# Kernel optimization log

Hardware: AMD Instinct MI355X
Metric: run time of the kernel (lower is better)

## Reference

```python
import jax, jax.numpy as jnp
import numpy as np

MODEL_DIM = 2048
NUM_HEADS = 16
NUM_KV_HEADS = 4
HEAD_DIM = MODEL_DIM // NUM_HEADS  # 128
ROPE_BASE = 10000.0
LOCAL_WINDOW = 1024
EPS = 1.1920929e-07  # torch.finfo(float32).eps, F.rms_norm default
NEG = -1e30


def setup_inputs() -> dict:
    key = jax.random.key(0)
    ks = jax.random.split(key, 5)
    s = 0.02
    return {
        "x": jax.random.normal(ks[0], (1, 4096, MODEL_DIM), jnp.float32),
        "Wq": jax.random.normal(ks[1], (MODEL_DIM, MODEL_DIM), jnp.float32) * s,
        "Wk": jax.random.normal(ks[2], (NUM_KV_HEADS * HEAD_DIM, MODEL_DIM), jnp.float32) * s,
        "Wv": jax.random.normal(ks[3], (NUM_KV_HEADS * HEAD_DIM, MODEL_DIM), jnp.float32) * s,
        "Wo": jax.random.normal(ks[4], (MODEL_DIM, MODEL_DIM), jnp.float32) * s,
    }


def _rms_norm(x):
    return x * jax.lax.rsqrt(jnp.mean(x * x, axis=-1, keepdims=True) + EPS)


def _rope_tables(seqlen, dtype):
    inv_freq = 1.0 / (ROPE_BASE ** (jnp.arange(0, HEAD_DIM, 2, dtype=jnp.float32) / HEAD_DIM))
    freqs = jnp.arange(seqlen, dtype=jnp.float32)[:, None] * inv_freq[None, :]  # [S, hd/2]
    return jnp.cos(freqs).astype(dtype), jnp.sin(freqs).astype(dtype)


def _apply_rope(x, cos, sin):
    # x: [B, H, S, hd]; cos/sin: [S, hd/2]
    half = x.shape[-1] // 2
    x1, x2 = x[..., :half], x[..., half:]
    c = cos[None, None, :, :]
    s = sin[None, None, :, :]
    return jnp.concatenate((x1 * c + x2 * s, x2 * c - x1 * s), axis=-1)


def reference(x, Wq, Wk, Wv, Wo):
    B, S, _ = x.shape
    G = NUM_HEADS // NUM_KV_HEADS
    q = (x @ Wq.T).reshape(B, S, NUM_HEADS, HEAD_DIM).transpose(0, 2, 1, 3)
    k = (x @ Wk.T).reshape(B, S, NUM_KV_HEADS, HEAD_DIM).transpose(0, 2, 1, 3)
    v = (x @ Wv.T).reshape(B, S, NUM_KV_HEADS, HEAD_DIM).transpose(0, 2, 1, 3)
    q = _rms_norm(q)
    k = _rms_norm(k)
    cos, sin = _rope_tables(S, q.dtype)
    q = _apply_rope(q, cos, sin)
    k = _apply_rope(k, cos, sin)
    # GQA: expand kv heads to match query heads
    k = jnp.repeat(k, G, axis=1)  # [B, H, S, hd]
    v = jnp.repeat(v, G, axis=1)
    scale = 1.0 / np.sqrt(HEAD_DIM)
    scores = jnp.einsum("bhqd,bhkd->bhqk", q, k) * scale  # [B, H, S, S]
    idx = jnp.arange(S)
    causal = idx[None, :] <= idx[:, None]
    in_window = idx[None, :] > idx[:, None] - LOCAL_WINDOW
    allowed = causal & in_window  # [S, S]
    scores = jnp.where(allowed[None, None, :, :], scores, NEG)
    probs = jax.nn.softmax(scores, axis=-1)
    y = jnp.einsum("bhqk,bhkd->bhqd", probs, v)  # [B, H, S, hd]
    y = y.transpose(0, 2, 1, 3).reshape(B, S, MODEL_DIM)
    return y @ Wo.T
```

## Files before the change

kernel.cpp:

```cpp
#include <hip/hip_runtime.h>

typedef short bf16x8 __attribute__((ext_vector_type(8)));
typedef float f32x4 __attribute__((ext_vector_type(4)));

__device__ __forceinline__ ushort f2b(float f) {
  union { float f; unsigned u; } v; v.f = f;
  unsigned r = v.u + 0x7FFF + ((v.u >> 16) & 1);
  return (ushort)(r >> 16);
}
__device__ __forceinline__ float b2f(ushort u) {
  union { unsigned u; float f; } v; v.u = ((unsigned)u) << 16;
  return v.f;
}
__device__ __forceinline__ unsigned cvtpk(float lo, float hi) {
  unsigned r;
  asm volatile("v_cvt_pk_bf16_f32 %0, %1, %2" : "=v"(r) : "v"(lo), "v"(hi));
  return r;
}
__device__ __forceinline__ f32x4 mfma16(bf16x8 a, bf16x8 b, f32x4 c) {
  return __builtin_amdgcn_mfma_f32_16x16x32_bf16(a, b, c, 0, 0, 0);
}

#define GLD_LDS16(g, l) \
  __builtin_amdgcn_global_load_lds((const __attribute__((address_space(1))) void*)(g), \
                                   (__attribute__((address_space(3))) void*)(l), 16, 0, 0)

__global__ __launch_bounds__(256) void cast_all(const float* __restrict__ x,
                                                const float* __restrict__ wq,
                                                const float* __restrict__ wk,
                                                const float* __restrict__ wv,
                                                const float* __restrict__ wo,
                                                ushort* __restrict__ xb,
                                                ushort* __restrict__ wqkvb,
                                                ushort* __restrict__ wob) {
  const long i = (long)blockIdx.x * 256 + threadIdx.x;
  const float* src;
  ushort* dst;
  long j;
  if (i < 2097152) {
    src = x; j = i; dst = xb;
  } else if (i < 3145728) {
    src = wq; j = i - 2097152; dst = wqkvb;
  } else if (i < 3407872) {
    src = wk; j = i - 3145728; dst = wqkvb + 4194304;
  } else if (i < 3670016) {
    src = wv; j = i - 3407872; dst = wqkvb + 5242880;
  } else {
    src = wo; j = i - 3670016; dst = wob;
  }
  float4 f = ((const float4*)src)[j];
  ushort4 u;
  u.x = f2b(f.x); u.y = f2b(f.y); u.z = f2b(f.z); u.w = f2b(f.w);
  ((ushort4*)dst)[j] = u;
}

__global__ void rope_tables_k(float* __restrict__ cosT, float* __restrict__ sinT) {
  int s = blockIdx.x, i = threadIdx.x;
  float inv = powf(10000.0f, -(float)i * (1.0f / 64.0f));
  float f = (float)s * inv;
  cosT[s * 64 + i] = cosf(f);
  sinT[s * 64 + i] = sinf(f);
}

template <int BM, int BN, bool BF16OUT>
__global__ __launch_bounds__(512, 2) void gemm8p(const ushort* __restrict__ A,
                                                 const ushort* __restrict__ B,
                                                 void* __restrict__ Cout,
                                                 int M, int N, int K) {
  constexpr int AF = BM / 64;
  constexpr int BF = BN / 64;
  constexpr int MFR = BM / 32;
  constexpr int LA = BM / 128;
  constexpr int LB = BN / 128;
  constexpr int ASZ = BM * 32;
  constexpr int BSZ = BN * 32;
  __shared__ __align__(16) ushort lds[4 * (ASZ + BSZ)];
  const int t = threadIdx.x;
  const int lane = t & 63, w = t >> 6;
  const int wr = w & 1, wc = w >> 1;
  const int l15 = lane & 15, l4 = lane >> 4;
  const int nbn = N / BN;
  const int nwg = (int)gridDim.x;
  int bid = (int)blockIdx.x;
  bid = (bid & 7) * (nwg >> 3) + (bid >> 3);
  const long m0 = (long)(bid / nbn) * BM;
  const long n0 = (long)(bid % nbn) * BN;
  const int nk = K >> 6;
  const int rdl = l15 * 32 + ((l4 ^ ((l15 >> 1) & 3)) * 8);

  f32x4 acc[MFR][BF] = {};
  bf16x8 af[AF], bf[BF];

#define STA(tile, ks)                                                          \
  do {                                                                         \
    const int tt_ = (tile) < nk ? (tile) : nk - 1;                             \
    _Pragma("unroll") for (int c = 0; c < LA; ++c) {                           \
      const int us_ = t * 8 + c * 4096;                                        \
      const int r_ = us_ >> 5;                                                 \
      const int cs_ = (((us_ >> 3) & 3) ^ ((r_ >> 1) & 3)) * 8;                \
      GLD_LDS16(A + (m0 + r_) * K + tt_ * 64 + (ks) * 32 + cs_,                \
                &lds[(((tile) & 1) * 2 + (ks)) * ASZ + us_]);                  \
    }                                                                          \
  } while (0)
#define STB(tile, ks)                                                          \
  do {                                                                         \
    const int tt_ = (tile) < nk ? (tile) : nk - 1;                             \
    _Pragma("unroll") for (int c = 0; c < LB; ++c) {                           \
      const int us_ = t * 8 + c * 4096;                                        \
      const int r_ = us_ >> 5;                                                 \
      const int cs_ = (((us_ >> 3) & 3) ^ ((r_ >> 1) & 3)) * 8;                \
      GLD_LDS16(B + (n0 + r_) * K + tt_ * 64 + (ks) * 32 + cs_,                \
                &lds[4 * ASZ + (((tile) & 1) * 2 + (ks)) * BSZ + us_]);        \
    }                                                                          \
  } while (0)
#define LDA8(slot, ks, mq)                                                     \
  _Pragma("unroll") for (int a = 0; a < AF; ++a)                               \
      af[a] = *(const bf16x8*)(&lds[((slot) * 2 + (ks)) * ASZ +                \
                                    (wr * MFR + (mq) * AF + a) * 512 + rdl]);
#define LDB8(slot, ks)                                                         \
  _Pragma("unroll") for (int b = 0; b < BF; ++b)                               \
      bf[b] = *(const bf16x8*)(&lds[4 * ASZ + ((slot) * 2 + (ks)) * BSZ +      \
                                    (wc * BF + b) * 512 + rdl]);
#define VMW()                                                                  \
  do {                                                                         \
    if constexpr (LA + 2 * LB == 6)                                            \
      asm volatile("s_waitcnt vmcnt(6)" ::: "memory");                         \
    else                                                                       \
      asm volatile("s_waitcnt vmcnt(5)" ::: "memory");                         \
  } while (0)
#define BARMM(mq)                                                              \
  do {                                                                         \
    __builtin_amdgcn_s_barrier();                                              \
    asm volatile("s_waitcnt lgkmcnt(0)" ::: "memory");                         \
    __builtin_amdgcn_sched_barrier(0);                                         \
    __builtin_amdgcn_s_setprio(1);                                             \
    _Pragma("unroll") for (int a = 0; a < AF; ++a)                             \
        _Pragma("unroll") for (int b = 0; b < BF; ++b)                         \
            acc[(mq) * AF + a][b] = mfma16(af[a], bf[b], acc[(mq) * AF + a][b]); \
    __builtin_amdgcn_s_setprio(0);                                             \
    __builtin_amdgcn_s_barrier();                                              \
  } while (0)

  STA(0, 0); STB(0, 0); STA(0, 1); STB(0, 1);
  STA(1, 0); STB(1, 0); STB(1, 1);
  VMW();
  __builtin_amdgcn_s_barrier();

  for (int i = 0; i < (nk >> 1); ++i) {
    const int t1 = 2 * i + 1, t2 = 2 * i + 2, t3 = 2 * i + 3;
    LDA8(0, 0, 0); LDB8(0, 0); STA(t1, 1);          BARMM(0);
    LDA8(0, 0, 1);             STB(t2, 0);          BARMM(1);
    LDA8(0, 1, 0); LDB8(0, 1); STA(t2, 0);          BARMM(0);
    LDA8(0, 1, 1);             STB(t2, 1); VMW();   BARMM(1);
    LDA8(1, 0, 0); LDB8(1, 0); STA(t2, 1);          BARMM(0);
    LDA8(1, 0, 1);             STB(t3, 0);          BARMM(1);
    LDA8(1, 1, 0); LDB8(1, 1); STA(t3, 0);          BARMM(0);
    LDA8(1, 1, 1);             STB(t3, 1); VMW();   BARMM(1);
  }
  asm volatile("s_waitcnt vmcnt(0)" ::: "memory");

#pragma unroll
  for (int m = 0; m < MFR; ++m) {
#pragma unroll
    for (int n = 0; n < BF; ++n) {
      long mrow = m0 + wr * (BM / 2) + m * 16 + l4 * 4;
      long ncol = n0 + wc * (BN / 4) + n * 16 + l15;
#pragma unroll
      for (int r = 0; r < 4; ++r) {
        if constexpr (BF16OUT)
          ((ushort*)Cout)[(mrow + r) * N + ncol] = f2b(acc[m][n][r]);
        else
          ((float*)Cout)[(mrow + r) * N + ncol] = acc[m][n][r];
      }
    }
  }
#undef STA
#undef STB
#undef LDA8
#undef LDB8
#undef VMW
#undef BARMM
}

__global__ __launch_bounds__(256) void postproc_k(const ushort* __restrict__ qkvb,
                                                  const float* __restrict__ cosT,
                                                  const float* __restrict__ sinT,
                                                  ushort* __restrict__ qb,
                                                  ushort* __restrict__ kb,
                                                  ushort* __restrict__ vtb) {
  const int lane = threadIdx.x & 63;
  const int s = blockIdx.x * 4 + (threadIdx.x >> 6);
  const int h = blockIdx.y;
  const int colbase = (h < 16) ? h * 128 : (h < 20 ? 2048 + (h - 16) * 128
                                                   : 2560 + (h - 20) * 128);
  const ushort* row = qkvb + (long)s * 3072 + colbase;
  float x1 = b2f(row[lane]), x2 = b2f(row[lane + 64]);
  if (h >= 20) {
    int kvh = h - 20;
    int spos = (s & ~31) | (((s >> 2) & 3) * 8 + ((s >> 4) & 1) * 4 + (s & 3));
    vtb[(long)(kvh * 128 + lane) * 4096 + spos]      = f2b(x1);
    vtb[(long)(kvh * 128 + lane + 64) * 4096 + spos] = f2b(x2);
    return;
  }
  float ss = x1 * x1 + x2 * x2;
#pragma unroll
  for (int m = 1; m < 64; m <<= 1) ss += __shfl_xor(ss, m);
  float rn = rsqrtf(ss * (1.0f / 128.0f) + 1.1920929e-07f);
  float c = cosT[s * 64 + lane], sn = sinT[s * 64 + lane];
  float x1n = x1 * rn, x2n = x2 * rn;
  float o1 = x1n * c + x2n * sn;
  float o2 = x2n * c - x1n * sn;
  if (h < 16) {
    const float scq = 0.08838834764831845f;
    ushort* dst = qb + ((long)h * 4096 + s) * 128;
    dst[lane] = f2b(o1 * scq);
    dst[lane + 64] = f2b(o2 * scq);
  } else {
    ushort* dst = kb + ((long)(h - 16) * 4096 + s) * 128;
    dst[lane] = f2b(o1);
    dst[lane + 64] = f2b(o2);
  }
}

__global__ __launch_bounds__(256, 2) void attn_k(const ushort* __restrict__ qb,
                                                 const ushort* __restrict__ kb,
                                                 const ushort* __restrict__ vtb,
                                                 ushort* __restrict__ yb) {
  __shared__ __align__(16) ushort lds[32768];
  const int t = threadIdx.x;
  const int lane = t & 63, w = t >> 6;
  const int l15 = lane & 15, l4 = lane >> 4;
  const int q0 = ((int)gridDim.x - 1 - (int)blockIdx.x) * 128;
  const int h = blockIdx.y, kvh = h >> 2;
  const int qw = q0 + w * 32;
  const int qA = qw + l15, qB = qw + 16 + l15;
  const int lrd = l15 * 32 + ((l4 ^ ((l15 >> 1) & 3)) * 8);

  bf16x8 qf0[4], qf1[4];
  {
    const ushort* QpA = qb + ((long)h * 4096 + qA) * 128 + l4 * 8;
    const ushort* QpB = qb + ((long)h * 4096 + qB) * 128 + l4 * 8;
#pragma unroll
    for (int c = 0; c < 4; ++c) {
      qf0[c] = *(const bf16x8*)(QpA + c * 32);
      qf1[c] = *(const bf16x8*)(QpB + c * 32);
    }
  }

  const ushort* Kg = kb + (long)kvh * 4096 * 128;
  const ushort* Vg = vtb + (long)kvh * 128 * 4096;

  int kb_lo = q0 - 1023; if (kb_lo < 0) kb_lo = 0; kb_lo &= ~63;
  const int nt = (q0 + 127 - kb_lo) / 64 + 1;

#define STAGE(kbs, b)                                                          \
  do {                                                                         \
    ushort* L_ = &lds[(b) * 16384];                                            \
    _Pragma("unroll") for (int c = 0; c < 8; ++c) {                            \
      const int us_ = t * 8 + c * 2048;                                        \
      if (c < 4) {                                                             \
        const int r_ = (us_ >> 5) & 63;                                        \
        const int cs_ = (((us_ >> 3) & 3) ^ ((r_ >> 1) & 3)) * 8;              \
        GLD_LDS16(Kg + (long)((kbs) + r_) * 128 + (us_ >> 11) * 32 + cs_,      \
                  L_ + us_);                                                   \
      } else {                                                                 \
        const int uv_ = us_ - 8192;                                            \
        const int r_ = (uv_ >> 5) & 127;                                       \
        const int cs_ = (((uv_ >> 3) & 3) ^ ((r_ >> 1) & 3)) * 8;              \
        GLD_LDS16(Vg + (long)r_ * 4096 + (kbs) + (uv_ >> 12) * 32 + cs_,       \
                  L_ + us_);                                                   \
      }                                                                        \
    }                                                                          \
  } while (0)

#define SMAX(sg, mr, lr, og, PA, PB)                                           \
  do {                                                                         \
    float mx = fmaxf(fmaxf(fmaxf(sg[0], sg[1]), fmaxf(sg[2], sg[3])),          \
                     fmaxf(fmaxf(sg[4], sg[5]), fmaxf(sg[6], sg[7])));         \
    mx = fmaxf(mx, fmaxf(fmaxf(fmaxf(sg[8], sg[9]), fmaxf(sg[10], sg[11])),    \
                         fmaxf(fmaxf(sg[12], sg[13]), fmaxf(sg[14], sg[15]))));\
    mx = fmaxf(mx, __shfl_xor(mx, 16));                                        \
    mx = fmaxf(mx, __shfl_xor(mx, 32));                                        \
    float mn;                                                                  \
    if (__all(mx <= (mr) + 8.0f)) {                                            \
      mn = (mr);                                                               \
    } else {                                                                   \
      mn = fmaxf((mr), mx);                                                    \
      const float corr = __expf((mr)-mn);                                      \
      (mr) = mn;                                                               \
      _Pragma("unroll") for (int db = 0; db < 8; ++db)                         \
          _Pragma("unroll") for (int r = 0; r < 4; ++r) og[db][r] *= corr;     \
      (lr) *= corr;                                                            \
    }                                                                          \
    float p[16];                                                               \
    _Pragma("unroll") for (int j = 0; j < 16; ++j) p[j] = __expf(sg[j] - mn);  \
    float ps = ((p[0] + p[1]) + (p[2] + p[3])) + ((p[4] + p[5]) + (p[6] + p[7])); \
    ps += ((p[8] + p[9]) + (p[10] + p[11])) + ((p[12] + p[13]) + (p[14] + p[15])); \
    ps += __shfl_xor(ps, 16);                                                  \
    ps += __shfl_xor(ps, 32);                                                  \
    (lr) += ps;                                                                \
    PA.u[0] = cvtpk(p[0], p[1]);   PA.u[1] = cvtpk(p[2], p[3]);                \
    PA.u[2] = cvtpk(p[4], p[5]);   PA.u[3] = cvtpk(p[6], p[7]);                \
    PB.u[0] = cvtpk(p[8], p[9]);   PB.u[1] = cvtpk(p[10], p[11]);              \
    PB.u[2] = cvtpk(p[12], p[13]); PB.u[3] = cvtpk(p[14], p[15]);              \
  } while (0)

  f32x4 o0[8] = {}, o1[8] = {};
  float mr0 = -1e30f, lr0 = 0.0f, mr1 = -1e30f, lr1 = 0.0f;

  STAGE(kb_lo, 0);
  asm volatile("s_waitcnt vmcnt(0)" ::: "memory");
  __syncthreads();

  for (int ti = 0; ti < nt; ++ti) {
    const int kbs = kb_lo + ti * 64;
    const int cur = ti & 1;
    if (ti + 1 < nt) STAGE(kbs + 64, cur ^ 1);

    if (kbs <= qw + 31 && kbs + 63 >= qw - 1023) {
      const ushort* Kl = &lds[cur * 16384];
      const ushort* Vl = Kl + 8192;

      f32x4 sc0[4], sc1[4];
#pragma unroll
      for (int st = 0; st < 4; ++st) {
        sc0[st] = f32x4{0.f, 0.f, 0.f, 0.f};
        sc1[st] = f32x4{0.f, 0.f, 0.f, 0.f};
#pragma unroll
        for (int c = 0; c < 4; ++c) {
          bf16x8 kf = *(const bf16x8*)(Kl + c * 2048 + st * 512 + lrd);
          sc0[st] = mfma16(kf, qf0[c], sc0[st]);
          sc1[st] = mfma16(kf, qf1[c], sc1[st]);
        }
      }

      float s0[16], s1[16];
      const bool fullA = (kbs + 64 <= qw) && (kbs >= qw - 1008);
      const bool fullB = (kbs + 64 <= qw + 16) && (kbs >= qw - 992);
      if (fullA) {
#pragma unroll
        for (int st = 0; st < 4; ++st)
#pragma unroll
          for (int r = 0; r < 4; ++r) s0[st * 4 + r] = sc0[st][r];
      } else {
#pragma unroll
        for (int st = 0; st < 4; ++st)
#pragma unroll
          for (int r = 0; r < 4; ++r) {
            const int ki = kbs + st * 16 + l4 * 4 + r;
            s0[st * 4 + r] = (ki <= qA && ki > qA - 1024) ? sc0[st][r] : -1e30f;
          }
      }
      if (fullB) {
#pragma unroll
        for (int st = 0; st < 4; ++st)
#pragma unroll
          for (int r = 0; r < 4; ++r) s1[st * 4 + r] = sc1[st][r];
      } else {
#pragma unroll
        for (int st = 0; st < 4; ++st)
#pragma unroll
          for (int r = 0; r < 4; ++r) {
            const int ki = kbs + st * 16 + l4 * 4 + r;
            s1[st * 4 + r] = (ki <= qB && ki > qB - 1024) ? sc1[st][r] : -1e30f;
          }
      }

      union { unsigned u[4]; bf16x8 v; } pa0, pb0, pa1, pb1;
      SMAX(s0, mr0, lr0, o0, pa0, pb0);
      SMAX(s1, mr1, lr1, o1, pa1, pb1);

#pragma unroll
      for (int db = 0; db < 8; ++db) {
        bf16x8 v0 = *(const bf16x8*)(Vl + db * 512 + lrd);
        o0[db] = mfma16(v0, pa0.v, o0[db]);
        o1[db] = mfma16(v0, pa1.v, o1[db]);
        bf16x8 v1 = *(const bf16x8*)(Vl + 4096 + db * 512 + lrd);
        o0[db] = mfma16(v1, pb0.v, o0[db]);
        o1[db] = mfma16(v1, pb1.v, o1[db]);
      }
    }
    __syncthreads();
  }

  const float i0 = 1.0f / lr0, i1 = 1.0f / lr1;
#pragma unroll
  for (int db = 0; db < 8; ++db)
#pragma unroll
    for (int r = 0; r < 4; ++r) {
      yb[(long)qA * 2048 + h * 128 + db * 16 + l4 * 4 + r] = f2b(o0[db][r] * i0);
      yb[(long)qB * 2048 + h * 128 + db * 16 + l4 * 4 + r] = f2b(o1[db][r] * i1);
    }
#undef STAGE
#undef SMAX
}

extern "C" void kernel_launch(void* const* d_in, const int* in_sizes, int n_in,
                              void* d_out, int out_size, void* d_ws, size_t ws_size,
                              hipStream_t stream) {
  (void)in_sizes; (void)n_in; (void)out_size; (void)ws_size;
  const float* x  = (const float*)d_in[0];
  const float* Wq = (const float*)d_in[1];
  const float* Wk = (const float*)d_in[2];
  const float* Wv = (const float*)d_in[3];
  const float* Wo = (const float*)d_in[4];
  const long S = 4096;
  ushort* ws   = (ushort*)d_ws;
  ushort* xb   = ws;
  ushort* wqkv = xb + S * 2048;
  ushort* wob  = wqkv + 3072L * 2048;
  ushort* qkvb = wob + 2048L * 2048;
  ushort* qb   = qkvb + S * 3072;
  ushort* kbuf = qb + S * 2048;
  ushort* vtb  = kbuf + 4L * 4096 * 128;
  ushort* yb   = vtb + 4L * 128 * 4096;
  float* cosT  = (float*)(yb + S * 2048);
  float* sinT  = cosT + S * 64;

  cast_all<<<dim3(18432), 256, 0, stream>>>(x, Wq, Wk, Wv, Wo, xb, wqkv, wob);
  gemm8p<256, 256, true><<<dim3(192), 512, 0, stream>>>(xb, wqkv, qkvb, 4096, 3072, 2048);
  rope_tables_k<<<dim3(4096), 64, 0, stream>>>(cosT, sinT);
  postproc_k<<<dim3(1024, 24), 256, 0, stream>>>(qkvb, cosT, sinT, qb, kbuf, vtb);
  attn_k<<<dim3(32, 16), 256, 0, stream>>>(qb, kbuf, vtb, yb);
  gemm8p<128, 256, false><<<dim3(256), 512, 0, stream>>>(yb, wob, d_out, 4096, 2048, 2048);
}
```

Measured before the change: 192.3 us.

## Replace LDS-staged K/V tiles with direct global fragment loads in attention

Removes the double-buffered global-to-LDS staging of K and V tiles and block-wide barriers; each wave now loads its MFMA fragments directly from global memory. The grid is flattened and remapped so heads sharing a KV head are scheduled together, aiming for L2 reuse, and the launch-bounds occupancy hint is dropped. This eliminates LDS traffic and syncs but makes each of the four waves re-read the same K/V data and removes the per-wave skip of fully masked tiles.

```diff
diff --git a/kernel.cpp b/kernel.cpp
--- a/kernel.cpp
+++ b/kernel.cpp
@@ -222,24 +222,25 @@
   }
 }
 
-__global__ __launch_bounds__(256, 2) void attn_k(const ushort* __restrict__ qb,
-                                                 const ushort* __restrict__ kb,
-                                                 const ushort* __restrict__ vtb,
-                                                 ushort* __restrict__ yb) {
-  __shared__ __align__(16) ushort lds[32768];
+__global__ __launch_bounds__(256) void attn_k(const ushort* __restrict__ qb,
+                                              const ushort* __restrict__ kb,
+                                              const ushort* __restrict__ vtb,
+                                              ushort* __restrict__ yb) {
   const int t = threadIdx.x;
   const int lane = t & 63, w = t >> 6;
   const int l15 = lane & 15, l4 = lane >> 4;
-  const int q0 = ((int)gridDim.x - 1 - (int)blockIdx.x) * 128;
-  const int h = blockIdx.y, kvh = h >> 2;
+  const int bid = (int)blockIdx.x;
+  const int h = (bid & 7) * 2 + ((bid >> 3) & 1);
+  const int gi = bid >> 4;
+  const int q0 = (31 - gi) * 128;
+  const int kvh = h >> 2;
   const int qw = q0 + w * 32;
   const int qA = qw + l15, qB = qw + 16 + l15;
-  const int lrd = l15 * 32 + ((l4 ^ ((l15 >> 1) & 3)) * 8);
 
   bf16x8 qf0[4], qf1[4];
   {
     const ushort* QpA = qb + ((long)h * 4096 + qA) * 128 + l4 * 8;
-    const ushort* QpB = qb + ((long)h * 4096 + qB) * 128 + l4 * 8;
+    const ushort* QpB = QpA + 16 * 128;
 #pragma unroll
     for (int c = 0; c < 4; ++c) {
       qf0[c] = *(const bf16x8*)(QpA + c * 32);
@@ -252,26 +253,6 @@
 
   int kb_lo = q0 - 1023; if (kb_lo < 0) kb_lo = 0; kb_lo &= ~63;
   const int nt = (q0 + 127 - kb_lo) / 64 + 1;
-
-#define STAGE(kbs, b)                                                          \
-  do {                                                                         \
-    ushort* L_ = &lds[(b) * 16384];                                            \
-    _Pragma("unroll") for (int c = 0; c < 8; ++c) {                            \
-      const int us_ = t * 8 + c * 2048;                                        \
-      if (c < 4) {                                                             \
-        const int r_ = (us_ >> 5) & 63;                                        \
-        const int cs_ = (((us_ >> 3) & 3) ^ ((r_ >> 1) & 3)) * 8;              \
-        GLD_LDS16(Kg + (long)((kbs) + r_) * 128 + (us_ >> 11) * 32 + cs_,      \
-                  L_ + us_);                                                   \
-      } else {                                                                 \
-        const int uv_ = us_ - 8192;                                            \
-        const int r_ = (uv_ >> 5) & 127;                                       \
-        const int cs_ = (((uv_ >> 3) & 3) ^ ((r_ >> 1) & 3)) * 8;              \
-        GLD_LDS16(Vg + (long)r_ * 4096 + (kbs) + (uv_ >> 12) * 32 + cs_,       \
-                  L_ + us_);                                                   \
-      }                                                                        \
-    }                                                                          \
-  } while (0)
 
 #define SMAX(sg, mr, lr, og, PA, PB)                                           \
   do {                                                                         \
@@ -308,79 +289,71 @@
   f32x4 o0[8] = {}, o1[8] = {};
   float mr0 = -1e30f, lr0 = 0.0f, mr1 = -1e30f, lr1 = 0.0f;
 
-  STAGE(kb_lo, 0);
-  asm volatile("s_waitcnt vmcnt(0)" ::: "memory");
-  __syncthreads();
-
   for (int ti = 0; ti < nt; ++ti) {
     const int kbs = kb_lo + ti * 64;
-    const int cur = ti & 1;
-    if (ti + 1 < nt) STAGE(kbs + 64, cur ^ 1);
-
-    if (kbs <= qw + 31 && kbs + 63 >= qw - 1023) {
-      const ushort* Kl = &lds[cur * 16384];
-      const ushort* Vl = Kl + 8192;
-
-      f32x4 sc0[4], sc1[4];
-#pragma unroll
-      for (int st = 0; st < 4; ++st) {
-        sc0[st] = f32x4{0.f, 0.f, 0.f, 0.f};
-        sc1[st] = f32x4{0.f, 0.f, 0.f, 0.f};
-#pragma unroll
-        for (int c = 0; c < 4; ++c) {
-          bf16x8 kf = *(const bf16x8*)(Kl + c * 2048 + st * 512 + lrd);
-          sc0[st] = mfma16(kf, qf0[c], sc0[st]);
-          sc1[st] = mfma16(kf, qf1[c], sc1[st]);
+
+    f32x4 sc0[4], sc1[4];
+#pragma unroll
+    for (int st = 0; st < 4; ++st) {
+      const ushort* kr = Kg + (long)(kbs + st * 16 + l15) * 128 + l4 * 8;
+      bf16x8 k0 = *(const bf16x8*)(kr);
+      bf16x8 k1 = *(const bf16x8*)(kr + 32);
+      bf16x8 k2 = *(const bf16x8*)(kr + 64);
+      bf16x8 k3 = *(const bf16x8*)(kr + 96);
+      f32x4 a0 = f32x4{0.f, 0.f, 0.f, 0.f}, a1 = a0;
+      a0 = mfma16(k0, qf0[0], a0); a1 = mfma16(k0, qf1[0], a1);
+      a0 = mfma16(k1, qf0[1], a0); a1 = mfma16(k1, qf1[1], a1);
+      a0 = mfma16(k2, qf0[2], a0); a1 = mfma16(k2, qf1[2], a1);
+      a0 = mfma16(k3, qf0[3], a0); a1 = mfma16(k3, qf1[3], a1);
+      sc0[st] = a0; sc1[st] = a1;
+    }
+
+    float s0[16], s1[16];
+    const bool fullA = (kbs + 64 <= qw) && (kbs >= qw - 1008);
+    const bool fullB = (kbs + 64 <= qw + 16) && (kbs >= qw - 992);
+    if (fullA) {
+#pragma unroll
+      for (int st = 0; st < 4; ++st)
+#pragma unroll
+        for (int r = 0; r < 4; ++r) s0[st * 4 + r] = sc0[st][r];
+    } else {
+#pragma unroll
+      for (int st = 0; st < 4; ++st)
+#pragma unroll
+        for (int r = 0; r < 4; ++r) {
+          const int ki = kbs + st * 16 + l4 * 4 + r;
+          s0[st * 4 + r] = (ki <= qA && ki > qA - 1024) ? sc0[st][r] : -1e30f;
         }
-      }
-
-      float s0[16], s1[16];
-      const bool fullA = (kbs + 64 <= qw) && (kbs >= qw - 1008);
-      const bool fullB = (kbs + 64 <= qw + 16) && (kbs >= qw - 992);
-      if (fullA) {
-#pragma unroll
-        for (int st = 0; st < 4; ++st)
-#pragma unroll
-          for (int r = 0; r < 4; ++r) s0[st * 4 + r] = sc0[st][r];
-      } else {
-#pragma unroll
-        for (int st = 0; st < 4; ++st)
-#pragma unroll
-          for (int r = 0; r < 4; ++r) {
-            const int ki = kbs + st * 16 + l4 * 4 + r;
-            s0[st * 4 + r] = (ki <= qA && ki > qA - 1024) ? sc0[st][r] : -1e30f;
-          }
-      }
-      if (fullB) {
-#pragma unroll
-        for (int st = 0; st < 4; ++st)
-#pragma unroll
-          for (int r = 0; r < 4; ++r) s1[st * 4 + r] = sc1[st][r];
-      } else {
-#pragma unroll
-        for (int st = 0; st < 4; ++st)
-#pragma unroll
-          for (int r = 0; r < 4; ++r) {
-            const int ki = kbs + st * 16 + l4 * 4 + r;
-            s1[st * 4 + r] = (ki <= qB && ki > qB - 1024) ? sc1[st][r] : -1e30f;
-          }
-      }
-
-      union { unsigned u[4]; bf16x8 v; } pa0, pb0, pa1, pb1;
-      SMAX(s0, mr0, lr0, o0, pa0, pb0);
-      SMAX(s1, mr1, lr1, o1, pa1, pb1);
-
-#pragma unroll
-      for (int db = 0; db < 8; ++db) {
-        bf16x8 v0 = *(const bf16x8*)(Vl + db * 512 + lrd);
-        o0[db] = mfma16(v0, pa0.v, o0[db]);
-        o1[db] = mfma16(v0, pa1.v, o1[db]);
-        bf16x8 v1 = *(const bf16x8*)(Vl + 4096 + db * 512 + lrd);
-        o0[db] = mfma16(v1, pb0.v, o0[db]);
-        o1[db] = mfma16(v1, pb1.v, o1[db]);
-      }
-    }
-    __syncthreads();
+    }
+    if (fullB) {
+#pragma unroll
+      for (int st = 0; st < 4; ++st)
+#pragma unroll
+        for (int r = 0; r < 4; ++r) s1[st * 4 + r] = sc1[st][r];
+    } else {
+#pragma unroll
+      for (int st = 0; st < 4; ++st)
+#pragma unroll
+        for (int r = 0; r < 4; ++r) {
+          const int ki = kbs + st * 16 + l4 * 4 + r;
+          s1[st * 4 + r] = (ki <= qB && ki > qB - 1024) ? sc1[st][r] : -1e30f;
+        }
+    }
+
+    union { unsigned u[4]; bf16x8 v; } pa0, pb0, pa1, pb1;
+    SMAX(s0, mr0, lr0, o0, pa0, pb0);
+    SMAX(s1, mr1, lr1, o1, pa1, pb1);
+
+#pragma unroll
+    for (int db = 0; db < 8; ++db) {
+      const ushort* vr = Vg + (long)(db * 16 + l15) * 4096 + kbs + l4 * 8;
+      bf16x8 v0 = *(const bf16x8*)(vr);
+      bf16x8 v1 = *(const bf16x8*)(vr + 32);
+      o0[db] = mfma16(v0, pa0.v, o0[db]);
+      o1[db] = mfma16(v0, pa1.v, o1[db]);
+      o0[db] = mfma16(v1, pb0.v, o0[db]);
+      o1[db] = mfma16(v1, pb1.v, o1[db]);
+    }
   }
 
   const float i0 = 1.0f / lr0, i1 = 1.0f / lr1;
@@ -391,7 +364,6 @@
       yb[(long)qA * 2048 + h * 128 + db * 16 + l4 * 4 + r] = f2b(o0[db][r] * i0);
       yb[(long)qB * 2048 + h * 128 + db * 16 + l4 * 4 + r] = f2b(o1[db][r] * i1);
     }
-#undef STAGE
 #undef SMAX
 }
 
@@ -421,6 +393,6 @@
   gemm8p<256, 256, true><<<dim3(192), 512, 0, stream>>>(xb, wqkv, qkvb, 4096, 3072, 2048);
   rope_tables_k<<<dim3(4096), 64, 0, stream>>>(cosT, sinT);
   postproc_k<<<dim3(1024, 24), 256, 0, stream>>>(qkvb, cosT, sinT, qb, kbuf, vtb);
-  attn_k<<<dim3(32, 16), 256, 0, stream>>>(qb, kbuf, vtb, yb);
+  attn_k<<<dim3(512), 256, 0, stream>>>(qb, kbuf, vtb, yb);
   gemm8p<128, 256, false><<<dim3(256), 512, 0, stream>>>(yb, wob, d_out, 4096, 2048, 2048);
 }
```

New measurement: 272.2 us. 41.5% more time.
